# Kernel tuning notes

Hardware: AMD Instinct MI355X
Metric: run time of the kernel (lower is better)

## Reference

```python
import jax, jax.numpy as jnp
import numpy as np

NUM_QUBITS = 11
STATE_SIZE = 2 ** NUM_QUBITS  # 2048
FUSION_DIM = 2048
THETA = np.pi / 4


def _apply_hadamards(state):
    # state: [B, 2**n] complex. Apply H to every qubit (qubit q <-> bit 2**q,
    # matching the original's little-endian index arithmetic).
    B, S = state.shape
    inv_sqrt2 = jnp.asarray(1.0 / np.sqrt(2.0), dtype=state.dtype)
    for q in range(NUM_QUBITS):
        # index = hi * 2**(q+1) + b * 2**q + lo
        s = state.reshape(B, S >> (q + 1), 2, 1 << q)
        a, b = s[:, :, 0, :], s[:, :, 1, :]
        s = jnp.stack([(a + b) * inv_sqrt2, (a - b) * inv_sqrt2], axis=2)
        state = s.reshape(B, S)
    return state


def _rz_diag():
    # RZ(theta) on every qubit is diagonal: phase exp(+i*theta/2) if bit set,
    # exp(-i*theta/2) otherwise -> total phase depends only on popcount.
    idx = jnp.arange(STATE_SIZE)
    bits = (idx[:, None] >> jnp.arange(NUM_QUBITS)[None, :]) & 1  # [S, n]
    popcount = bits.sum(axis=-1).astype(jnp.float32)
    phase = (THETA / 2.0) * (2.0 * popcount - NUM_QUBITS)
    return jnp.exp(1j * phase).astype(jnp.complex64)  # [S]


def setup_inputs() -> dict:
    key = jax.random.key(0)
    k1, k2 = jax.random.split(key)
    x1 = jax.random.normal(k1, (8192, 1024), dtype=jnp.float32)
    x2 = jax.random.normal(k2, (8192, 1024), dtype=jnp.float32)
    return {"x1": x1, "x2": x2}


def reference(x1, x2):
    combined = jnp.concatenate([x1, x2], axis=-1)  # [B, D]
    B, D = combined.shape
    m = min(D, STATE_SIZE)
    # _prepare_quantum_state: embed first min(D, 2**n) features as complex amplitudes
    state = jnp.zeros((B, STATE_SIZE), dtype=jnp.complex64)
    state = state.at[:, :m].set(combined[:, :m].astype(jnp.complex64))
    # H on every qubit
    state = _apply_hadamards(state)
    # CNOT chain: the original swaps each (i, i^target) pair twice -> identity.
    # Faithfully reproduced as a no-op.
    # RZ on every qubit (diagonal phase)
    state = state * _rz_diag()[None, :]
    # _measure_quantum_state: probabilities, then pad/truncate to fusion_dim
    feats = (jnp.abs(state) ** 2).astype(jnp.float32)  # [B, 2**n]
    if feats.shape[1] < FUSION_DIM:
        feats = jnp.pad(feats, ((0, 0), (0, FUSION_DIM - feats.shape[1])))
    elif feats.shape[1] > FUSION_DIM:
        feats = feats[:, :FUSION_DIM]
    return feats
```

## Files before the change

kernel.cpp:

```cpp
#include <hip/hip_runtime.h>


template <int CTRL>
__device__ __forceinline__ float dpp_xmov(float x) {
    return __int_as_float(__builtin_amdgcn_update_dpp(
        0, __float_as_int(x), CTRL, 0xF, 0xF, true));
}

__global__ __launch_bounds__(256) void qf_wht_kernel(const float* __restrict__ x1,
                                                     const float* __restrict__ x2,
                                                     float* __restrict__ out,
                                                     int nrows) {
    const int wave = threadIdx.x >> 6;
    const int lane = threadIdx.x & 63;
    const int row  = blockIdx.x * 4 + wave;
    if (row >= nrows) return;

    float v[32];

    const float* __restrict__ p1 = x1 + (size_t)row * 1024 + lane * 4;
    const float* __restrict__ p2 = x2 + (size_t)row * 1024 + lane * 4;
#pragma unroll
    for (int jo = 0; jo < 4; ++jo) {
        float4 f = *(const float4*)(p1 + jo * 256);
        v[jo * 4 + 0] = f.x; v[jo * 4 + 1] = f.y;
        v[jo * 4 + 2] = f.z; v[jo * 4 + 3] = f.w;
    }
#pragma unroll
    for (int jo = 4; jo < 8; ++jo) {
        float4 f = *(const float4*)(p2 + (jo - 4) * 256);
        v[jo * 4 + 0] = f.x; v[jo * 4 + 1] = f.y;
        v[jo * 4 + 2] = f.z; v[jo * 4 + 3] = f.w;
    }

#pragma unroll
    for (int m = 1; m < 32; m <<= 1) {
#pragma unroll
        for (int j = 0; j < 32; ++j) {
            if ((j & m) == 0) {
                const float a = v[j];
                const float b = v[j | m];
                v[j]     = a + b;
                v[j | m] = a - b;
            }
        }
    }

    {
        const float s = (lane & 1) ? -1.0f : 1.0f;
#pragma unroll
        for (int j = 0; j < 32; ++j) {
            const float p = dpp_xmov<0xB1>(v[j]);
            v[j] = fmaf(s, v[j], p);
        }
    }
    {
        const float s = (lane & 2) ? -1.0f : 1.0f;
#pragma unroll
        for (int j = 0; j < 32; ++j) {
            const float p = dpp_xmov<0x4E>(v[j]);
            v[j] = fmaf(s, v[j], p);
        }
    }
    {
        const float s = (lane & 4) ? -1.0f : 1.0f;
#pragma unroll
        for (int j = 0; j < 32; ++j) {
            const float p = dpp_xmov<0x141>(dpp_xmov<0x1B>(v[j]));
            v[j] = fmaf(s, v[j], p);
        }
    }
    {
        const float s = (lane & 8) ? -1.0f : 1.0f;
#pragma unroll
        for (int j = 0; j < 32; ++j) {
            const float p = dpp_xmov<0x140>(dpp_xmov<0x141>(v[j]));
            v[j] = fmaf(s, v[j], p);
        }
    }
    {
        const float s = (lane & 16) ? -1.0f : 1.0f;
#pragma unroll
        for (int j = 0; j < 32; ++j) {
            const float p = __int_as_float(
                __builtin_amdgcn_ds_swizzle(__float_as_int(v[j]), 0x401F));
            v[j] = fmaf(s, v[j], p);
        }
    }
    {
        const float s = (lane & 32) ? -1.0f : 1.0f;
        const int idx32 = (lane ^ 32) << 2;
#pragma unroll
        for (int j = 0; j < 32; ++j) {
            const float p = __int_as_float(
                __builtin_amdgcn_ds_bpermute(idx32, __float_as_int(v[j])));
            v[j] = fmaf(s, v[j], p);
        }
    }

    const float scale = 1.0f / 2048.0f;
    float* __restrict__ po = out + (size_t)row * 2048 + lane * 4;
#pragma unroll
    for (int jo = 0; jo < 8; ++jo) {
        float4 f;
        f.x = v[jo * 4 + 0] * v[jo * 4 + 0] * scale;
        f.y = v[jo * 4 + 1] * v[jo * 4 + 1] * scale;
        f.z = v[jo * 4 + 2] * v[jo * 4 + 2] * scale;
        f.w = v[jo * 4 + 3] * v[jo * 4 + 3] * scale;
        *(float4*)(po + jo * 256) = f;
    }
}

extern "C" void kernel_launch(void* const* d_in, const int* in_sizes, int n_in,
                              void* d_out, int out_size, void* d_ws, size_t ws_size,
                              hipStream_t stream) {
    const float* x1 = (const float*)d_in[0];
    const float* x2 = (const float*)d_in[1];
    float* out = (float*)d_out;

    const int nrows = in_sizes[0] / 1024;
    const int blocks = (nrows + 3) / 4;
    qf_wht_kernel<<<blocks, 256, 0, stream>>>(x1, x2, out, nrows);
}
```

Baseline: 111.7 us.

## Restructure WHT stages per load chunk and use permlane32 swap with nontemporal IO

Reorders the Walsh-Hadamard butterflies so that each 4-float load chunk gets its in-register stages and all cross-lane stages (DPP, swizzle, and a permlane32_swap pair replacing ds_bpermute) right after it arrives. The remaining register stages then run over the full 32-value array. The intent is to overlap cross-lane shuffle latency with outstanding loads and to avoid the LDS-routed bpermute. Loads and stores become nontemporal to reduce cache pollution on this streaming kernel. The xor-32 stage now needs two permlane swaps per value pair.

```diff
diff --git a/kernel.cpp b/kernel.cpp
--- a/kernel.cpp
+++ b/kernel.cpp
@@ -1,10 +1,37 @@
 #include <hip/hip_runtime.h>
 
+
+typedef float f32x4 __attribute__((ext_vector_type(4)));
+typedef unsigned int u32x2 __attribute__((ext_vector_type(2)));
 
 template <int CTRL>
 __device__ __forceinline__ float dpp_xmov(float x) {
     return __int_as_float(__builtin_amdgcn_update_dpp(
         0, __float_as_int(x), CTRL, 0xF, 0xF, true));
+}
+
+__device__ __forceinline__ float lane_chain(float x, float s1, float s2,
+                                            float s4, float s8, float s16) {
+    x = fmaf(s1, x, dpp_xmov<0xB1>(x));
+    x = fmaf(s2, x, dpp_xmov<0x4E>(x));
+    x = fmaf(s4, x, dpp_xmov<0x141>(dpp_xmov<0x1B>(x)));
+    x = fmaf(s8, x, dpp_xmov<0x140>(dpp_xmov<0x141>(x)));
+    x = fmaf(s16, x, __int_as_float(
+            __builtin_amdgcn_ds_swizzle(__float_as_int(x), 0x401F)));
+    return x;
+}
+
+__device__ __forceinline__ void xor32_pair(float& x, float& y) {
+    u32x2 r = __builtin_amdgcn_permlane32_swap(
+        __float_as_uint(x), __float_as_uint(y), false, false);
+    const float lo = __uint_as_float(r[0]);
+    const float hi = __uint_as_float(r[1]);
+    const float a = lo + hi;
+    const float b = lo - hi;
+    u32x2 r2 = __builtin_amdgcn_permlane32_swap(
+        __float_as_uint(a), __float_as_uint(b), false, false);
+    x = __uint_as_float(r2[0]);
+    y = __uint_as_float(r2[1]);
 }
 
 __global__ __launch_bounds__(256) void qf_wht_kernel(const float* __restrict__ x1,
@@ -16,25 +43,52 @@
     const int row  = blockIdx.x * 4 + wave;
     if (row >= nrows) return;
 
-    float v[32];
+    const float s1  = (lane & 1)  ? -1.0f : 1.0f;
+    const float s2  = (lane & 2)  ? -1.0f : 1.0f;
+    const float s4  = (lane & 4)  ? -1.0f : 1.0f;
+    const float s8  = (lane & 8)  ? -1.0f : 1.0f;
+    const float s16 = (lane & 16) ? -1.0f : 1.0f;
 
     const float* __restrict__ p1 = x1 + (size_t)row * 1024 + lane * 4;
     const float* __restrict__ p2 = x2 + (size_t)row * 1024 + lane * 4;
+    f32x4 f[8];
 #pragma unroll
-    for (int jo = 0; jo < 4; ++jo) {
-        float4 f = *(const float4*)(p1 + jo * 256);
-        v[jo * 4 + 0] = f.x; v[jo * 4 + 1] = f.y;
-        v[jo * 4 + 2] = f.z; v[jo * 4 + 3] = f.w;
-    }
+    for (int jo = 0; jo < 4; ++jo)
+        f[jo] = __builtin_nontemporal_load(
+            reinterpret_cast<const f32x4*>(p1 + jo * 256));
 #pragma unroll
-    for (int jo = 4; jo < 8; ++jo) {
-        float4 f = *(const float4*)(p2 + (jo - 4) * 256);
-        v[jo * 4 + 0] = f.x; v[jo * 4 + 1] = f.y;
-        v[jo * 4 + 2] = f.z; v[jo * 4 + 3] = f.w;
+    for (int jo = 4; jo < 8; ++jo)
+        f[jo] = __builtin_nontemporal_load(
+            reinterpret_cast<const f32x4*>(p2 + (jo - 4) * 256));
+
+    float v[32];
+#pragma unroll
+    for (int jo = 0; jo < 8; ++jo) {
+        const float a01 = f[jo][0] + f[jo][1];
+        const float d01 = f[jo][0] - f[jo][1];
+        const float a23 = f[jo][2] + f[jo][3];
+        const float d23 = f[jo][2] - f[jo][3];
+        float c0 = a01 + a23;
+        float c1 = d01 + d23;
+        float c2 = a01 - a23;
+        float c3 = d01 - d23;
+
+        c0 = lane_chain(c0, s1, s2, s4, s8, s16);
+        c1 = lane_chain(c1, s1, s2, s4, s8, s16);
+        c2 = lane_chain(c2, s1, s2, s4, s8, s16);
+        c3 = lane_chain(c3, s1, s2, s4, s8, s16);
+
+        xor32_pair(c0, c1);
+        xor32_pair(c2, c3);
+
+        v[jo * 4 + 0] = c0;
+        v[jo * 4 + 1] = c1;
+        v[jo * 4 + 2] = c2;
+        v[jo * 4 + 3] = c3;
     }
 
 #pragma unroll
-    for (int m = 1; m < 32; m <<= 1) {
+    for (int m = 4; m <= 16; m <<= 1) {
 #pragma unroll
         for (int j = 0; j < 32; ++j) {
             if ((j & m) == 0) {
@@ -46,68 +100,16 @@
         }
     }
 
-    {
-        const float s = (lane & 1) ? -1.0f : 1.0f;
-#pragma unroll
-        for (int j = 0; j < 32; ++j) {
-            const float p = dpp_xmov<0xB1>(v[j]);
-            v[j] = fmaf(s, v[j], p);
-        }
-    }
-    {
-        const float s = (lane & 2) ? -1.0f : 1.0f;
-#pragma unroll
-        for (int j = 0; j < 32; ++j) {
-            const float p = dpp_xmov<0x4E>(v[j]);
-            v[j] = fmaf(s, v[j], p);
-        }
-    }
-    {
-        const float s = (lane & 4) ? -1.0f : 1.0f;
-#pragma unroll
-        for (int j = 0; j < 32; ++j) {
-            const float p = dpp_xmov<0x141>(dpp_xmov<0x1B>(v[j]));
-            v[j] = fmaf(s, v[j], p);
-        }
-    }
-    {
-        const float s = (lane & 8) ? -1.0f : 1.0f;
-#pragma unroll
-        for (int j = 0; j < 32; ++j) {
-            const float p = dpp_xmov<0x140>(dpp_xmov<0x141>(v[j]));
-            v[j] = fmaf(s, v[j], p);
-        }
-    }
-    {
-        const float s = (lane & 16) ? -1.0f : 1.0f;
-#pragma unroll
-        for (int j = 0; j < 32; ++j) {
-            const float p = __int_as_float(
-                __builtin_amdgcn_ds_swizzle(__float_as_int(v[j]), 0x401F));
-            v[j] = fmaf(s, v[j], p);
-        }
-    }
-    {
-        const float s = (lane & 32) ? -1.0f : 1.0f;
-        const int idx32 = (lane ^ 32) << 2;
-#pragma unroll
-        for (int j = 0; j < 32; ++j) {
-            const float p = __int_as_float(
-                __builtin_amdgcn_ds_bpermute(idx32, __float_as_int(v[j])));
-            v[j] = fmaf(s, v[j], p);
-        }
-    }
-
     const float scale = 1.0f / 2048.0f;
     float* __restrict__ po = out + (size_t)row * 2048 + lane * 4;
 #pragma unroll
     for (int jo = 0; jo < 8; ++jo) {
-        float4 f;
-        f.x = v[jo * 4 + 0] * v[jo * 4 + 0] * scale;
-        f.y = v[jo * 4 + 1] * v[jo * 4 + 1] * scale;
-        f.z = v[jo * 4 + 2] * v[jo * 4 + 2] * scale;
-        f.w = v[jo * 4 + 3] * v[jo * 4 + 3] * scale;
-        *(float4*)(po + jo * 256) = f;
+        f32x4 o;
+        o[0] = v[jo * 4 + 0] * v[jo * 4 + 0] * scale;
+        o[1] = v[jo * 4 + 1] * v[jo * 4 + 1] * scale;
+        o[2] = v[jo * 4 + 2] * v[jo * 4 + 2] * scale;
+        o[3] = v[jo * 4 + 3] * v[jo * 4 + 3] * scale;
+        __builtin_nontemporal_store(o, reinterpret_cast<f32x4*>(po + jo * 256));
     }
 }
 
```

Measured after the change: 116.3 us. 4.1% more time.
